# Optimization experiments

Measured on AMD Instinct MI355X. Metric: run time of the kernel, lower is better.

The kernel has to match this reference:

```python
import jax, jax.numpy as jnp
import numpy as np

N_NODES = 50000
N_EDGES = 800000
D_IN = 128
D_OUT = 128
ALPHA = 0.5


def setup_inputs() -> dict:
    key = jax.random.key(0)
    k1, k2, k3, k4, k5, k6 = jax.random.split(key, 6)
    x = jax.random.normal(k1, (N_NODES, D_IN), dtype=jnp.float32)
    edge_index = jax.random.randint(k2, (2, N_EDGES), 0, N_NODES, dtype=jnp.int32)
    s = 1.0 / np.sqrt(D_IN)  # torch.nn.Linear default init bound
    W_src = jax.random.uniform(k3, (D_IN, D_OUT), jnp.float32, -s, s)
    b_src = jax.random.uniform(k4, (D_OUT,), jnp.float32, -s, s)
    W_dst = jax.random.uniform(k5, (D_IN, D_OUT), jnp.float32, -s, s)
    b_dst = jax.random.uniform(k6, (D_OUT,), jnp.float32, -s, s)
    return {"x": x, "edge_index": edge_index, "W_src": W_src, "b_src": b_src,
            "W_dst": W_dst, "b_dst": b_dst}


def reference(x, edge_index, W_src, b_src, W_dst, b_dst):
    row, col = edge_index[0], edge_index[1]
    ones = jnp.ones((row.shape[0],), dtype=x.dtype)
    # out-degree = row sums of A; in-degree = column sums of A
    out_deg = jax.ops.segment_sum(ones, row, num_segments=N_NODES)
    in_deg = jax.ops.segment_sum(ones, col, num_segments=N_NODES)
    d_out = jnp.where(out_deg > 0, out_deg ** -0.5, 0.0)
    d_in = jnp.where(in_deg > 0, in_deg ** -0.5, 0.0)
    # D_out^{-1/2} A D_in^{-1/2}: per-edge weight. For A^T the normalized
    # weight at (col,row) is d_in[col]*d_out[row] == same weight, transposed scatter.
    w = d_out[row] * d_in[col]  # [E]
    msg_fwd = w[:, None] * x[col]  # [E, D_IN]
    agg_fwd = jax.ops.segment_sum(msg_fwd, row, num_segments=N_NODES)  # adj_norm @ x
    msg_bwd = w[:, None] * x[row]
    agg_bwd = jax.ops.segment_sum(msg_bwd, col, num_segments=N_NODES)  # adj_t_norm @ x
    out = ALPHA * (agg_fwd @ W_src + b_src) + (1.0 - ALPHA) * (agg_bwd @ W_dst + b_dst)
    return out
```

## Files before the change

### kernel.cpp

```cpp
#include <hip/hip_runtime.h>
#include <hip/hip_bf16.h>


constexpr int N_NODES = 50000;
constexpr int N_EDGES = 800000;
constexpr int D = 128;
constexpr int CAP = 48;
constexpr int NPBK = 512;
constexpr int NBUK = (N_NODES + NPBK - 1) / NPBK;
constexpr int ECH = 8192;
constexpr int NCH = (N_EDGES + ECH - 1) / ECH;
constexpr int CAPB = 12288;

typedef __bf16 bf16x8 __attribute__((ext_vector_type(8)));
typedef float  f32x4  __attribute__((ext_vector_type(4)));

__global__ __launch_bounds__(256) void k_part(const int* __restrict__ row,
                                              const int* __restrict__ col,
                                              int* __restrict__ tail,
                                              unsigned* __restrict__ part) {
    __shared__ int cnt[NBUK], base[NBUK], pos[NBUK];
    const int dir = blockIdx.x & 1;
    const int chunk = blockIdx.x >> 1;
    const int* dst = dir ? col : row;
    const int* src = dir ? row : col;
    for (int i = threadIdx.x; i < NBUK; i += 256) { cnt[i] = 0; pos[i] = 0; }
    __syncthreads();
    const int e0 = chunk * ECH;
    const int e1 = min(e0 + ECH, N_EDGES);
    for (int e = e0 + threadIdx.x; e < e1; e += 256)
        atomicAdd(&cnt[dst[e] >> 9], 1);
    __syncthreads();
    for (int i = threadIdx.x; i < NBUK; i += 256)
        base[i] = (cnt[i] > 0) ? atomicAdd(&tail[dir * NBUK + i], cnt[i]) : 0;
    __syncthreads();
    for (int e = e0 + threadIdx.x; e < e1; e += 256) {
        int d = dst[e], s = src[e];
        int b = d >> 9;
        int p = base[b] + atomicAdd(&pos[b], 1);
        if (p < CAPB)
            part[((size_t)dir * NBUK + b) * CAPB + p] =
                ((unsigned)(d & (NPBK - 1)) << 16) | (unsigned)s;
    }
}

__global__ __launch_bounds__(256) void k_bin(const int* __restrict__ tail,
                                             const unsigned* __restrict__ part,
                                             unsigned short* __restrict__ binF,
                                             unsigned short* __restrict__ binB,
                                             int* __restrict__ cntF,
                                             int* __restrict__ cntB) {
    __shared__ alignas(16) unsigned short bins[NPBK * CAP];
    __shared__ int cnt[NPBK];
    const int dir = blockIdx.x & 1;
    const int b = blockIdx.x >> 1;
    for (int i = threadIdx.x; i < NPBK; i += 256) cnt[i] = 0;
    __syncthreads();
    const int n = min(tail[dir * NBUK + b], CAPB);
    const unsigned* p = &part[((size_t)dir * NBUK + b) * CAPB];
    for (int i = threadIdx.x; i < n; i += 256) {
        unsigned ent = p[i];
        int dl = ent >> 16;
        int q = atomicAdd(&cnt[dl], 1);
        if (q < CAP) bins[dl * CAP + q] = (unsigned short)(ent & 0xFFFFu);
    }
    __syncthreads();
    unsigned short* gbin = dir ? binB : binF;
    int* gcnt = dir ? cntB : cntF;
    const int node0 = b * NPBK;
    const int nv = min(NPBK, N_NODES - node0);
    const int nq = nv * (CAP * 2 / 16);
    const uint4* bw = (const uint4*)bins;
    uint4* gw = (uint4*)&gbin[(size_t)node0 * CAP];
    for (int i = threadIdx.x; i < nq; i += 256) gw[i] = bw[i];
    for (int i = threadIdx.x; i < nv; i += 256) gcnt[node0 + i] = cnt[i];
}

__global__ __launch_bounds__(256) void k_aux(const int* __restrict__ cntF,
                                             const int* __restrict__ cntB,
                                             float* __restrict__ sc_row,
                                             float* __restrict__ sc_col,
                                             const float* __restrict__ Wsrc,
                                             const float* __restrict__ Wdst,
                                             __hip_bfloat16* __restrict__ Wpk) {
    const int NB_DINV = (N_NODES + 255) / 256;
    if (blockIdx.x < NB_DINV) {
        int i = blockIdx.x * 256 + threadIdx.x;
        if (i < N_NODES) {
            int a = cntF[i];
            sc_row[i] = (a > 0) ? rsqrtf((float)a) : 0.f;
            int b = cntB[i];
            sc_col[i] = (b > 0) ? rsqrtf((float)b) : 0.f;
        }
        return;
    }
    int tid = (blockIdx.x - NB_DINV) * 256 + threadIdx.x;
    int f = tid >> 6;
    int lane = tid & 63;
    int dir = f >> 5;
    int ct = (f >> 2) & 7;
    int ks = f & 3;
    const float* W = dir ? Wdst : Wsrc;
    int k0 = ks * 32 + (lane >> 4) * 8;
    int n = ct * 16 + (lane & 15);
    __hip_bfloat16 v[8];
    #pragma unroll
    for (int j = 0; j < 8; ++j) v[j] = __float2bfloat16(W[(k0 + j) * D + n]);
    *(bf16x8*)&Wpk[(size_t)tid * 8] = *(const bf16x8*)v;
}

__global__ __launch_bounds__(256) void k_gemm_mfma(const float* __restrict__ x,
                                                   const bf16x8* __restrict__ Wpk,
                                                   const float* __restrict__ sc_col,
                                                   const float* __restrict__ sc_row,
                                                   __hip_bfloat16* __restrict__ hF,
                                                   __hip_bfloat16* __restrict__ hB) {
    const int wave = threadIdx.x >> 6;
    const int lane = threadIdx.x & 63;
    const int quad = lane >> 4;
    const int m0 = blockIdx.x * 64 + wave * 16;

    const int arow = min(m0 + (lane & 15), N_NODES - 1);
    bf16x8 a[4];
    #pragma unroll
    for (int ks = 0; ks < 4; ++ks) {
        const float* px = &x[(size_t)arow * D + ks * 32 + quad * 8];
        float4 v0 = *(const float4*)px;
        float4 v1 = *(const float4*)(px + 4);
        union { bf16x8 v; __hip_bfloat16 e[8]; } u;
        u.e[0] = __float2bfloat16(v0.x); u.e[1] = __float2bfloat16(v0.y);
        u.e[2] = __float2bfloat16(v0.z); u.e[3] = __float2bfloat16(v0.w);
        u.e[4] = __float2bfloat16(v1.x); u.e[5] = __float2bfloat16(v1.y);
        u.e[6] = __float2bfloat16(v1.z); u.e[7] = __float2bfloat16(v1.w);
        a[ks] = u.v;
    }

    const int crow = m0 + quad * 4;
    float fF[4], fB[4];
    #pragma unroll
    for (int r = 0; r < 4; ++r) {
        int nd = min(crow + r, N_NODES - 1);
        fF[r] = 0.5f * sc_col[nd];
        fB[r] = 0.5f * sc_row[nd];
    }

    const bf16x8* WpkF = Wpk;
    const bf16x8* WpkB = Wpk + 32 * 64;

    #pragma unroll
    for (int ct = 0; ct < 8; ++ct) {
        f32x4 cF = {0.f, 0.f, 0.f, 0.f};
        f32x4 cB = {0.f, 0.f, 0.f, 0.f};
        #pragma unroll
        for (int ks = 0; ks < 4; ++ks) {
            bf16x8 bF = WpkF[(ct * 4 + ks) * 64 + lane];
            bf16x8 bB = WpkB[(ct * 4 + ks) * 64 + lane];
            cF = __builtin_amdgcn_mfma_f32_16x16x32_bf16(a[ks], bF, cF, 0, 0, 0);
            cB = __builtin_amdgcn_mfma_f32_16x16x32_bf16(a[ks], bB, cB, 0, 0, 0);
        }
        const int colb = ct * 16 + (lane & 15);
        #pragma unroll
        for (int r = 0; r < 4; ++r) {
            int nd = crow + r;
            if (nd < N_NODES) {
                hF[(size_t)nd * D + colb] = __float2bfloat16(fF[r] * cF[r]);
                hB[(size_t)nd * D + colb] = __float2bfloat16(fB[r] * cB[r]);
            }
        }
    }
}

__device__ __forceinline__ float4 bf4_to_f4(uint2 u) {
    union { unsigned i; float f; } a, b, c, d;
    a.i = u.x << 16;
    b.i = u.x & 0xFFFF0000u;
    c.i = u.y << 16;
    d.i = u.y & 0xFFFF0000u;
    return make_float4(a.f, b.f, c.f, d.f);
}

__global__ __launch_bounds__(256) void k_gather(const unsigned short* __restrict__ binF,
                                                const int* __restrict__ cntF,
                                                const unsigned short* __restrict__ binB,
                                                const int* __restrict__ cntB,
                                                const float* __restrict__ sc_row,
                                                const float* __restrict__ sc_col,
                                                const uint2* __restrict__ hF,
                                                const uint2* __restrict__ hB,
                                                const float* __restrict__ b_src,
                                                const float* __restrict__ b_dst,
                                                float* __restrict__ out) {
    const int node = blockIdx.x * 4 + (threadIdx.x >> 6);
    const int lane = threadIdx.x & 63;
    const int half = lane >> 5;
    const int l32 = lane & 31;
    const int nF = min(cntF[node], CAP);
    const int nB = min(cntB[node], CAP);

    int entF = (lane < nF) ? (int)binF[(size_t)node * CAP + lane] : 0;
    int entB = (lane < nB) ? (int)binB[(size_t)node * CAP + lane] : 0;

    const int sTailF = __shfl(entF, (nF > 0) ? nF - 1 : 0);
    const int sTailB = __shfl(entB, (nB > 0) ? nB - 1 : 0);

    float4 accF = make_float4(0.f, 0.f, 0.f, 0.f);
    {
        const int npair = nF >> 1;
        int i = 0;
        for (; i + 3 < npair; i += 4) {
            int s0 = __shfl(entF, 2 * i + half);
            int s1 = __shfl(entF, 2 * (i + 1) + half);
            int s2 = __shfl(entF, 2 * (i + 2) + half);
            int s3 = __shfl(entF, 2 * (i + 3) + half);
            uint2 v0 = hF[(size_t)s0 * 32 + l32];
            uint2 v1 = hF[(size_t)s1 * 32 + l32];
            uint2 v2 = hF[(size_t)s2 * 32 + l32];
            uint2 v3 = hF[(size_t)s3 * 32 + l32];
            float4 f0 = bf4_to_f4(v0), f1 = bf4_to_f4(v1);
            float4 f2 = bf4_to_f4(v2), f3 = bf4_to_f4(v3);
            accF.x += (f0.x + f1.x) + (f2.x + f3.x);
            accF.y += (f0.y + f1.y) + (f2.y + f3.y);
            accF.z += (f0.z + f1.z) + (f2.z + f3.z);
            accF.w += (f0.w + f1.w) + (f2.w + f3.w);
        }
        for (; i < npair; ++i) {
            int s = __shfl(entF, 2 * i + half);
            float4 f = bf4_to_f4(hF[(size_t)s * 32 + l32]);
            accF.x += f.x; accF.y += f.y; accF.z += f.z; accF.w += f.w;
        }
        if ((nF & 1) && half == 0) {
            float4 f = bf4_to_f4(hF[(size_t)sTailF * 32 + l32]);
            accF.x += f.x; accF.y += f.y; accF.z += f.z; accF.w += f.w;
        }
    }
    float4 accB = make_float4(0.f, 0.f, 0.f, 0.f);
    {
        const int npair = nB >> 1;
        int i = 0;
        for (; i + 3 < npair; i += 4) {
            int s0 = __shfl(entB, 2 * i + half);
            int s1 = __shfl(entB, 2 * (i + 1) + half);
            int s2 = __shfl(entB, 2 * (i + 2) + half);
            int s3 = __shfl(entB, 2 * (i + 3) + half);
            uint2 v0 = hB[(size_t)s0 * 32 + l32];
            uint2 v1 = hB[(size_t)s1 * 32 + l32];
            uint2 v2 = hB[(size_t)s2 * 32 + l32];
            uint2 v3 = hB[(size_t)s3 * 32 + l32];
            float4 f0 = bf4_to_f4(v0), f1 = bf4_to_f4(v1);
            float4 f2 = bf4_to_f4(v2), f3 = bf4_to_f4(v3);
            accB.x += (f0.x + f1.x) + (f2.x + f3.x);
            accB.y += (f0.y + f1.y) + (f2.y + f3.y);
            accB.z += (f0.z + f1.z) + (f2.z + f3.z);
            accB.w += (f0.w + f1.w) + (f2.w + f3.w);
        }
        for (; i < npair; ++i) {
            int s = __shfl(entB, 2 * i + half);
            float4 f = bf4_to_f4(hB[(size_t)s * 32 + l32]);
            accB.x += f.x; accB.y += f.y; accB.z += f.z; accB.w += f.w;
        }
        if ((nB & 1) && half == 0) {
            float4 f = bf4_to_f4(hB[(size_t)sTailB * 32 + l32]);
            accB.x += f.x; accB.y += f.y; accB.z += f.z; accB.w += f.w;
        }
    }

    accF.x += __shfl_xor(accF.x, 32);
    accF.y += __shfl_xor(accF.y, 32);
    accF.z += __shfl_xor(accF.z, 32);
    accF.w += __shfl_xor(accF.w, 32);
    accB.x += __shfl_xor(accB.x, 32);
    accB.y += __shfl_xor(accB.y, 32);
    accB.z += __shfl_xor(accB.z, 32);
    accB.w += __shfl_xor(accB.w, 32);

    if (half == 0) {
        float4 bs = *(const float4*)&b_src[l32 * 4];
        float4 bd = *(const float4*)&b_dst[l32 * 4];
        float sF = sc_row[node];
        float sB = sc_col[node];
        float4 o;
        o.x = 0.5f * (bs.x + bd.x) + sF * accF.x + sB * accB.x;
        o.y = 0.5f * (bs.y + bd.y) + sF * accF.y + sB * accB.y;
        o.z = 0.5f * (bs.z + bd.z) + sF * accF.z + sB * accB.z;
        o.w = 0.5f * (bs.w + bd.w) + sF * accF.w + sB * accB.w;
        *(float4*)&out[(size_t)node * D + l32 * 4] = o;
    }
}

extern "C" void kernel_launch(void* const* d_in, const int* in_sizes, int n_in,
                              void* d_out, int out_size, void* d_ws, size_t ws_size,
                              hipStream_t stream) {
    const float* x     = (const float*)d_in[0];
    const int*   edges = (const int*)d_in[1];
    const float* W_src = (const float*)d_in[2];
    const float* b_src = (const float*)d_in[3];
    const float* W_dst = (const float*)d_in[4];
    const float* b_dst = (const float*)d_in[5];
    float* out = (float*)d_out;

    const int* row = edges;
    const int* col = edges + N_EDGES;

    __hip_bfloat16* hFu    = (__hip_bfloat16*)d_ws;
    __hip_bfloat16* hBu    = hFu + (size_t)N_NODES * D;
    __hip_bfloat16* Wpk    = hBu + (size_t)N_NODES * D;
    float*          sc_row = (float*)(Wpk + 64 * 512);
    float*          sc_col = sc_row + N_NODES;
    int*            cntF   = (int*)(sc_col + N_NODES);
    int*            cntB   = cntF + N_NODES;
    int*            tail   = cntB + N_NODES;
    unsigned*       part   = (unsigned*)(tail + 256);
    unsigned short* binF   = (unsigned short*)(part + (size_t)2 * NBUK * CAPB);
    unsigned short* binB   = binF + (size_t)N_NODES * CAP;

    (void)hipMemsetAsync(tail, 0, 256 * sizeof(int), stream);

    const int gP = NCH * 2;
    const int gB = NBUK * 2;
    const int gN = (N_NODES + 255) / 256;
    const int gA = gN + 16;
    const int gM = (N_NODES + 63) / 64;
    const int gG = N_NODES / 4;

    k_part<<<gP, 256, 0, stream>>>(row, col, tail, part);
    k_bin<<<gB, 256, 0, stream>>>(tail, part, binF, binB, cntF, cntB);
    k_aux<<<gA, 256, 0, stream>>>(cntF, cntB, sc_row, sc_col, W_src, W_dst, Wpk);
    k_gemm_mfma<<<gM, 256, 0, stream>>>(x, (const bf16x8*)Wpk, sc_col, sc_row, hFu, hBu);
    k_gather<<<gG, 256, 0, stream>>>(binF, cntF, binB, cntB, sc_row, sc_col,
                                     (const uint2*)hFu, (const uint2*)hBu,
                                     b_src, b_dst, out);
}
```

Before: 199.9 us.

## Fold aux kernel into partition and bin kernels, stage weights in LDS

Removes the separate k_aux launch: the weight bf16 packing moves into extra blocks of k_part, and the degree rsqrt scaling is computed directly in k_bin where counts are already in shared memory. The edge chunk size shrinks so more partition blocks run in parallel. The GEMM kernel now copies the packed weights (64 KB) into LDS once per block instead of reading them from global memory per MFMA. This saves one launch and a pass over the count arrays, in exchange for more global atomics on tail and a large LDS footprint per GEMM block, which may lower occupancy.

```diff
diff --git a/kernel.cpp b/kernel.cpp
--- a/kernel.cpp
+++ b/kernel.cpp
@@ -8,7 +8,7 @@
 constexpr int CAP = 48;
 constexpr int NPBK = 512;
 constexpr int NBUK = (N_NODES + NPBK - 1) / NPBK;
-constexpr int ECH = 8192;
+constexpr int ECH = 2048;
 constexpr int NCH = (N_EDGES + ECH - 1) / ECH;
 constexpr int CAPB = 12288;
 
@@ -18,10 +18,30 @@
 __global__ __launch_bounds__(256) void k_part(const int* __restrict__ row,
                                               const int* __restrict__ col,
                                               int* __restrict__ tail,
-                                              unsigned* __restrict__ part) {
+                                              unsigned* __restrict__ part,
+                                              const float* __restrict__ Wsrc,
+                                              const float* __restrict__ Wdst,
+                                              __hip_bfloat16* __restrict__ Wpk) {
+    const int bid = blockIdx.x;
+    if (bid >= NCH * 2) {
+        int tid = (bid - NCH * 2) * 256 + threadIdx.x;
+        int f = tid >> 6;
+        int lane = tid & 63;
+        int dir = f >> 5;
+        int ct = (f >> 2) & 7;
+        int ks = f & 3;
+        const float* W = dir ? Wdst : Wsrc;
+        int k0 = ks * 32 + (lane >> 4) * 8;
+        int n = ct * 16 + (lane & 15);
+        __hip_bfloat16 v[8];
+        #pragma unroll
+        for (int j = 0; j < 8; ++j) v[j] = __float2bfloat16(W[(k0 + j) * D + n]);
+        *(bf16x8*)&Wpk[(size_t)tid * 8] = *(const bf16x8*)v;
+        return;
+    }
     __shared__ int cnt[NBUK], base[NBUK], pos[NBUK];
-    const int dir = blockIdx.x & 1;
-    const int chunk = blockIdx.x >> 1;
+    const int dir = bid & 1;
+    const int chunk = bid >> 1;
     const int* dst = dir ? col : row;
     const int* src = dir ? row : col;
     for (int i = threadIdx.x; i < NBUK; i += 256) { cnt[i] = 0; pos[i] = 0; }
@@ -49,7 +69,9 @@
                                              unsigned short* __restrict__ binF,
                                              unsigned short* __restrict__ binB,
                                              int* __restrict__ cntF,
-                                             int* __restrict__ cntB) {
+                                             int* __restrict__ cntB,
+                                             float* __restrict__ sc_row,
+                                             float* __restrict__ sc_col) {
     __shared__ alignas(16) unsigned short bins[NPBK * CAP];
     __shared__ int cnt[NPBK];
     const int dir = blockIdx.x & 1;
@@ -67,46 +89,18 @@
     __syncthreads();
     unsigned short* gbin = dir ? binB : binF;
     int* gcnt = dir ? cntB : cntF;
+    float* sc = dir ? sc_col : sc_row;
     const int node0 = b * NPBK;
     const int nv = min(NPBK, N_NODES - node0);
     const int nq = nv * (CAP * 2 / 16);
     const uint4* bw = (const uint4*)bins;
     uint4* gw = (uint4*)&gbin[(size_t)node0 * CAP];
     for (int i = threadIdx.x; i < nq; i += 256) gw[i] = bw[i];
-    for (int i = threadIdx.x; i < nv; i += 256) gcnt[node0 + i] = cnt[i];
-}
-
-__global__ __launch_bounds__(256) void k_aux(const int* __restrict__ cntF,
-                                             const int* __restrict__ cntB,
-                                             float* __restrict__ sc_row,
-                                             float* __restrict__ sc_col,
-                                             const float* __restrict__ Wsrc,
-                                             const float* __restrict__ Wdst,
-                                             __hip_bfloat16* __restrict__ Wpk) {
-    const int NB_DINV = (N_NODES + 255) / 256;
-    if (blockIdx.x < NB_DINV) {
-        int i = blockIdx.x * 256 + threadIdx.x;
-        if (i < N_NODES) {
-            int a = cntF[i];
-            sc_row[i] = (a > 0) ? rsqrtf((float)a) : 0.f;
-            int b = cntB[i];
-            sc_col[i] = (b > 0) ? rsqrtf((float)b) : 0.f;
-        }
-        return;
-    }
-    int tid = (blockIdx.x - NB_DINV) * 256 + threadIdx.x;
-    int f = tid >> 6;
-    int lane = tid & 63;
-    int dir = f >> 5;
-    int ct = (f >> 2) & 7;
-    int ks = f & 3;
-    const float* W = dir ? Wdst : Wsrc;
-    int k0 = ks * 32 + (lane >> 4) * 8;
-    int n = ct * 16 + (lane & 15);
-    __hip_bfloat16 v[8];
-    #pragma unroll
-    for (int j = 0; j < 8; ++j) v[j] = __float2bfloat16(W[(k0 + j) * D + n]);
-    *(bf16x8*)&Wpk[(size_t)tid * 8] = *(const bf16x8*)v;
+    for (int i = threadIdx.x; i < nv; i += 256) {
+        int c = cnt[i];
+        gcnt[node0 + i] = c;
+        sc[node0 + i] = (c > 0) ? rsqrtf((float)c) : 0.f;
+    }
 }
 
 __global__ __launch_bounds__(256) void k_gemm_mfma(const float* __restrict__ x,
@@ -115,6 +109,9 @@
                                                    const float* __restrict__ sc_row,
                                                    __hip_bfloat16* __restrict__ hF,
                                                    __hip_bfloat16* __restrict__ hB) {
+    __shared__ bf16x8 Bs[64 * 64];
+    for (int i = threadIdx.x; i < 64 * 64; i += 256) Bs[i] = Wpk[i];
+
     const int wave = threadIdx.x >> 6;
     const int lane = threadIdx.x & 63;
     const int quad = lane >> 4;
@@ -144,8 +141,7 @@
         fB[r] = 0.5f * sc_row[nd];
     }
 
-    const bf16x8* WpkF = Wpk;
-    const bf16x8* WpkB = Wpk + 32 * 64;
+    __syncthreads();
 
     #pragma unroll
     for (int ct = 0; ct < 8; ++ct) {
@@ -153,8 +149,8 @@
         f32x4 cB = {0.f, 0.f, 0.f, 0.f};
         #pragma unroll
         for (int ks = 0; ks < 4; ++ks) {
-            bf16x8 bF = WpkF[(ct * 4 + ks) * 64 + lane];
-            bf16x8 bB = WpkB[(ct * 4 + ks) * 64 + lane];
+            bf16x8 bF = Bs[(ct * 4 + ks) * 64 + lane];
+            bf16x8 bB = Bs[(32 + ct * 4 + ks) * 64 + lane];
             cF = __builtin_amdgcn_mfma_f32_16x16x32_bf16(a[ks], bF, cF, 0, 0, 0);
             cB = __builtin_amdgcn_mfma_f32_16x16x32_bf16(a[ks], bB, cB, 0, 0, 0);
         }
@@ -315,16 +311,13 @@
 
     (void)hipMemsetAsync(tail, 0, 256 * sizeof(int), stream);
 
-    const int gP = NCH * 2;
+    const int gP = NCH * 2 + 16;
     const int gB = NBUK * 2;
-    const int gN = (N_NODES + 255) / 256;
-    const int gA = gN + 16;
     const int gM = (N_NODES + 63) / 64;
     const int gG = N_NODES / 4;
 
-    k_part<<<gP, 256, 0, stream>>>(row, col, tail, part);
-    k_bin<<<gB, 256, 0, stream>>>(tail, part, binF, binB, cntF, cntB);
-    k_aux<<<gA, 256, 0, stream>>>(cntF, cntB, sc_row, sc_col, W_src, W_dst, Wpk);
+    k_part<<<gP, 256, 0, stream>>>(row, col, tail, part, W_src, W_dst, Wpk);
+    k_bin<<<gB, 256, 0, stream>>>(tail, part, binF, binB, cntF, cntB, sc_row, sc_col);
     k_gemm_mfma<<<gM, 256, 0, stream>>>(x, (const bf16x8*)Wpk, sc_col, sc_row, hFu, hBu);
     k_gather<<<gG, 256, 0, stream>>>(binF, cntF, binB, cntB, sc_row, sc_col,
                                      (const uint2*)hFu, (const uint2*)hBu,
```

Result: no change. 197.1 us (-1.4%).
